# Performance work log

Measured on AMD Instinct MI355X. Metric: run time of the kernel, lower is better.

The kernel has to match this reference:

```python
import jax, jax.numpy as jnp
from jax import lax
import numpy as np

L, G, C = 4, 2, 4  # num_blocks, num_sparsity_groups, num_sparsity_cardinals
IMAGE_MEAN = 0.5
SCALE = 2


def _wn(v, g):
    # weight_norm over dims (1,2,3), g per output channel
    n = jnp.sqrt(jnp.sum(v * v, axis=(1, 2, 3), keepdims=True))
    return (g.reshape(-1, 1, 1, 1) / n) * v


def _conv(x, w, b, pad):
    y = lax.conv_general_dilated(x, w, (1, 1), [(pad, pad), (pad, pad)],
                                 dimension_numbers=('NCHW', 'OIHW', 'NCHW'))
    return y + b[None, :, None, None]


def _dyn_conv(x, v, g, b, mw, mb):
    # sparsity-routed conv: per-sample expert mixture of kernels
    w = _wn(v, g)                                   # [G*out, in, k, k]
    B = x.shape[0]
    logits = x.mean((-1, -2)) @ mw.T + mb           # [B, G*C]
    s = jax.nn.softmax(logits.reshape(B, G, C), axis=1)
    wv = w.reshape(G, C, -1, *w.shape[1:])          # [G, C, D, in, k, k]
    wper = jnp.einsum('bgc,gcdikl->bcdikl', s, wv)
    wper = wper.reshape(B, -1, *w.shape[1:])        # [B, out, in, k, k]
    bper = jnp.einsum('bgc,gcd->bcd', s, b.reshape(G, C, -1)).reshape(B, -1)

    def per_sample(xi, wi, bi):
        yi = lax.conv_general_dilated(xi[None], wi, (1, 1), [(1, 1), (1, 1)],
                                      dimension_numbers=('NCHW', 'OIHW', 'NCHW'))[0]
        return yi + bi[:, None, None]

    return jax.vmap(per_sample)(x, wper, bper)


def _pixel_shuffle(x, r):
    B, Cc, H, W = x.shape
    x = x.reshape(B, Cc // (r * r), r, r, H, W)
    x = x.transpose(0, 1, 4, 2, 5, 3)
    return x.reshape(B, Cc // (r * r), H * r, W * r)


def setup_inputs() -> dict:
    key = jax.random.key(0)
    ks = jax.random.split(key, 16)
    f32 = jnp.float32
    inp = {
        'x': jax.random.uniform(ks[0], (8, 3, 64, 64), dtype=f32),
        'head_v': jax.random.normal(ks[1], (64, 3, 3, 3), dtype=f32) * 0.05,
        'head_g': jnp.ones((64,), f32),
        'head_b': jnp.zeros((64,), f32),
        'b1_v': jax.random.normal(ks[2], (L, 512, 64, 3, 3), dtype=f32) * 0.05,
        'b1_g': jnp.full((L, 512), 2.0, f32),
        'b1_b': jnp.zeros((L, 512), f32),
        'b1_mw': jax.random.normal(ks[3], (L, 8, 64), dtype=f32) * 0.05,
        'b1_mb': jax.random.normal(ks[4], (L, 8), dtype=f32) * 0.05,
        'b2_v': jax.random.normal(ks[5], (L, 128, 256, 3, 3), dtype=f32) * 0.05,
        'b2_g': jnp.full((L, 128), 1.0 / np.sqrt(L), f32),
        'b2_b': jnp.zeros((L, 128), f32),
        'b2_mw': jax.random.normal(ks[6], (L, 8, 256), dtype=f32) * 0.05,
        'b2_mb': jax.random.normal(ks[7], (L, 8), dtype=f32) * 0.05,
        'tail_v': jax.random.normal(ks[8], (12, 64, 3, 3), dtype=f32) * 0.05,
        'tail_g': jnp.ones((12,), f32),
        'tail_b': jnp.zeros((12,), f32),
        'skip_v': jax.random.normal(ks[9], (12, 3, 5, 5), dtype=f32) * 0.05,
        'skip_g': jnp.ones((12,), f32),
        'skip_b': jnp.zeros((12,), f32),
    }
    return inp


def reference(x, head_v, head_g, head_b,
              b1_v, b1_g, b1_b, b1_mw, b1_mb,
              b2_v, b2_g, b2_b, b2_mw, b2_mb,
              tail_v, tail_g, tail_b,
              skip_v, skip_g, skip_b):
    x = x - IMAGE_MEAN
    h = _conv(x, _wn(head_v, head_g), head_b, pad=1)
    for l in range(L):
        r0 = h
        t = _dyn_conv(h, b1_v[l], b1_g[l], b1_b[l], b1_mw[l], b1_mb[l])
        t = jax.nn.relu(t)
        t = _dyn_conv(t, b2_v[l], b2_g[l], b2_b[l], b2_mw[l], b2_mb[l])
        h = t + r0
    body = _conv(h, _wn(tail_v, tail_g), tail_b, pad=1)
    s = _conv(x, _wn(skip_v, skip_g), skip_b, pad=2)
    y = _pixel_shuffle(body + s, SCALE) + IMAGE_MEAN
    return y
```

## Files before the change

### kernel.cpp

```cpp
#include <hip/hip_runtime.h>

typedef __attribute__((ext_vector_type(8))) short bf16x8;
typedef __attribute__((ext_vector_type(4))) float f32x4;
typedef __attribute__((ext_vector_type(4))) unsigned short u16x4;
typedef __attribute__((ext_vector_type(8))) unsigned short u16x8;

__device__ __forceinline__ unsigned short bf16u(float x) {
    unsigned int u = __builtin_bit_cast(unsigned int, x);
    unsigned int r = (u + 0x7fffu + ((u >> 16) & 1u)) >> 16;
    return (unsigned short)r;
}
__device__ __forceinline__ void gll16(const void* g, void* l) {
    __builtin_amdgcn_global_load_lds((const __attribute__((address_space(1))) void*)g,
                                     (__attribute__((address_space(3))) void*)l, 16, 0, 0);
}

__global__ __launch_bounds__(256) void zero_all(unsigned short* __restrict__ hbf,
                                                unsigned short* __restrict__ tbf,
                                                float* __restrict__ sums) {
    int i = blockIdx.x * 256 + threadIdx.x;
    u16x8 z8 = {0, 0, 0, 0, 0, 0, 0, 0};
    if (i < 16640) {
        int chv = i & 7, pb = i >> 3, pos = pb % 260, b = pb / 260;
        int y, x;
        if (pos < 66) { y = 0; x = pos; }
        else if (pos < 132) { y = 65; x = pos - 66; }
        else if (pos < 196) { y = pos - 131; x = 0; }
        else { y = pos - 195; x = 65; }
        *(u16x8*)&hbf[(((size_t)b * 66 + y) * 66 + x) * 64 + chv * 8] = z8;
    } else if (i < 83200) {
        int j = i - 16640;
        int chv = j & 7, pb = j >> 3;
        int pos = pb % 260, bc = pb / 260;
        int y, x;
        if (pos < 66) { y = 0; x = pos; }
        else if (pos < 132) { y = 65; x = pos - 66; }
        else if (pos < 196) { y = pos - 131; x = 0; }
        else { y = pos - 195; x = 65; }
        *(u16x8*)&tbf[(((size_t)bc * 66 + y) * 66 + x) * 64 + chv * 8] = z8;
    } else {
        int k = i - 83200;
        f32x4 z4 = {0.f, 0.f, 0.f, 0.f};
        ((f32x4*)sums)[k] = z4;
    }
}

__global__ __launch_bounds__(256) void wn_all(
    const float* __restrict__ hv, const float* __restrict__ hg, float* __restrict__ hw,
    const float* __restrict__ tv, const float* __restrict__ tg, float* __restrict__ tw,
    const float* __restrict__ kv, const float* __restrict__ kg, float* __restrict__ kw,
    const float* __restrict__ b1v, const float* __restrict__ b1g, float* __restrict__ b1s,
    const float* __restrict__ b2v, const float* __restrict__ b2g, float* __restrict__ b2s) {
    int blk = blockIdx.x;
    const float *v, *g;
    float *outw = nullptr, *outs = nullptr;
    int len, row;
    if (blk < 64)        { v = hv;  g = hg;  outw = hw;  len = 27;   row = blk; }
    else if (blk < 76)   { v = tv;  g = tg;  outw = tw;  len = 576;  row = blk - 64; }
    else if (blk < 88)   { v = kv;  g = kg;  outw = kw;  len = 75;   row = blk - 76; }
    else if (blk < 2136) { v = b1v; g = b1g; outs = b1s; len = 576;  row = blk - 88; }
    else                 { v = b2v; g = b2g; outs = b2s; len = 2304; row = blk - 2136; }

    __shared__ float red[4];
    __shared__ float s_sc;
    const float* vr = v + (size_t)row * len;
    float ss = 0.f;
    for (int i = threadIdx.x; i < len; i += 256) { float a = vr[i]; ss += a * a; }
    for (int o = 32; o > 0; o >>= 1) ss += __shfl_down(ss, o);
    if ((threadIdx.x & 63) == 0) red[threadIdx.x >> 6] = ss;
    __syncthreads();
    if (threadIdx.x == 0) s_sc = g[row] / sqrtf(red[0] + red[1] + red[2] + red[3]);
    __syncthreads();
    float sc = s_sc;
    if (outs) {
        if (threadIdx.x == 0) outs[row] = sc;
    } else {
        float* orow = outw + (size_t)row * len;
        for (int i = threadIdx.x; i < len; i += 256) orow[i] = vr[i] * sc;
    }
}

template <int IC, int GOC, int LGG>
__global__ __launch_bounds__(256) void combine_v2(
    const float* __restrict__ v, const float* __restrict__ scale,
    const float* __restrict__ msum, const float* __restrict__ mw,
    const float* __restrict__ mb, float* __restrict__ s_out,
    unsigned short* __restrict__ wq, int D, int OC) {
    constexpr int ROWF = IC * 9;
    constexpr int KCh = IC / 32;
    constexpr int TOTC = GOC * KCh * 9 * 4;
    __shared__ float lv[2 * GOC * ROWF];
    __shared__ float lg[8], sv8[8];
    int tid = threadIdx.x;
    int b = blockIdx.y, ocg = blockIdx.x * GOC;
    {
        int j = tid >> 5, l32 = tid & 31;
        float part = 0.f;
        for (int i = l32; i < IC; i += 32) part += msum[b * IC + i] * mw[j * IC + i];
        for (int m = 16; m > 0; m >>= 1) part += __shfl_xor(part, m);
        if (l32 == 0) lg[j] = part * (1.f / 4096.f) + mb[j];
    }
    for (int i = tid; i < 2 * GOC * ROWF; i += 256) {
        int r = i / ROWF, jj = i - r * ROWF;
        int oc_r = (r / GOC) * OC + ocg + (r % GOC);
        lv[i] = v[(size_t)oc_r * ROWF + jj] * scale[oc_r];
    }
    __syncthreads();
    if (tid < 8) {
        int g = tid >> 2, c = tid & 3;
        float l0 = lg[c], l1 = lg[4 + c];
        float m = fmaxf(l0, l1);
        float e0 = __expf(l0 - m), e1 = __expf(l1 - m);
        float val = ((g == 0) ? e0 : e1) / (e0 + e1);
        sv8[tid] = val;
        if (blockIdx.x == 0) s_out[b * 8 + tid] = val;
    }
    __syncthreads();
    for (int ci = tid; ci < TOTC; ci += 256) {
        int ml = ci & (GOC - 1);
        int c = ci >> LGG;
        int kg = c & 3, c2 = c >> 2;
        int t = c2 % 9, kc = c2 / 9;
        int oc = ocg + ml;
        int cd = oc / D;
        float s0 = sv8[cd], s1 = sv8[4 + cd];
        const float* p0 = &lv[(size_t)ml * ROWF];
        const float* p1 = &lv[(size_t)(GOC + ml) * ROWF];
        u16x8 pk;
#pragma unroll
        for (int kj = 0; kj < 8; ++kj) {
            int ic9 = (kc * 32 + kg * 8 + kj) * 9 + t;
            pk[kj] = bf16u(s0 * p0[ic9] + s1 * p1[ic9]);
        }
        int ot = oc >> 6, mo = oc & 63;
        size_t w_off = ((((size_t)(b * (OC >> 6) + ot) * KCh + kc) * 9 + t) * 4 + kg) * 512 + mo * 8;
        *(u16x8*)&wq[w_off] = pk;
    }
}

__global__ void tail_repack(const float* __restrict__ tw, unsigned short* __restrict__ wq) {
    int idx = blockIdx.x * 256 + threadIdx.x;
    int kj = idx & 7;
    int tmp = idx >> 3;
    int mo = tmp % 16; tmp /= 16;
    int kg = tmp & 3; tmp >>= 2;
    int t = tmp % 9; tmp /= 9;
    int kc = tmp;
    int ic = kc * 32 + kg * 8 + kj;
    float val = (mo < 12) ? tw[((size_t)mo * 64 + ic) * 9 + t] : 0.f;
    wq[idx] = bf16u(val);
}

template <int IC, int OC, int MT, int WM, int WN, int NR,
          bool RELU, bool RES, bool WF32, bool WBF, int OCR, bool DYNB>
__global__ __launch_bounds__(256) void conv_mfma(
    const unsigned short* __restrict__ in_bf,
    const unsigned short* __restrict__ wq,
    const float* __restrict__ bias_raw, const float* __restrict__ s8, int lgD,
    const float* __restrict__ res, float* __restrict__ out,
    unsigned short* __restrict__ out_bf, float* __restrict__ msum, long wstride) {
    constexpr int KCH = IC / 32;
    constexpr int NRH = NR + 2;
    constexpr int NT = NR * 64;
    constexpr int NF = (NT / 16) / WN;
    constexpr int MW = MT / (16 * WM);
    constexpr int WELEM = 9 * 32 * MT;
    constexpr int SELEM = NRH * 66 * 32;
    constexpr int WCH = WELEM / 8;
    constexpr int SCH = SELEM / 8;
    constexpr int OCB = (OCR % 64 == 0) ? OCR / 64 : 1;

    __shared__ __align__(16) unsigned short S[2][SELEM];
    __shared__ __align__(16) unsigned short W[2][WELEM];
    __shared__ float MRED[WN][MT];

    const int b = blockIdx.z, ot = blockIdx.y;
    const int y0 = blockIdx.x * NR;
    const int tid = threadIdx.x;
    const int lane = tid & 63;
    const int wid = tid >> 6;
    const int wm = wid / WN, wn = wid % WN;
    const int l15 = lane & 15, lk = lane >> 4;
    const int wmo = wm * (MT / WM);
    const int wno = wn * (NT / WN);

    f32x4 acc[MW][NF];
#pragma unroll
    for (int mf = 0; mf < MW; ++mf)
#pragma unroll
        for (int nf = 0; nf < NF; ++nf)
#pragma unroll
            for (int q = 0; q < 4; ++q) acc[mf][nf][q] = 0.f;

    const unsigned short* inb = in_bf + (size_t)b * (IC / 64) * 4356 * 64;
    const unsigned short* wqb = wq + (size_t)b * wstride + (size_t)ot * (KCH * WELEM);

    auto STAGE = [&](int kc, int buf) {
        const unsigned short* wsrc = wqb + (size_t)kc * WELEM;
        for (int i = tid; i < WCH; i += 256)
            gll16(wsrc + i * 8, (char*)W[buf] + i * 16);
        const unsigned short* sb = inb + (size_t)(kc >> 1) * (4356 * 64) + (kc & 1) * 32;
        for (int i = tid; i < SCH; i += 256) {
            int Lz = i ^ ((i >> 3) & 7);
            int lk2 = Lz & 3, cr = Lz >> 2;
            int col = cr % 66, row = cr / 66;
            gll16(sb + ((size_t)(y0 + row) * 66 + col) * 64 + lk2 * 8,
                  (char*)S[buf] + i * 16);
        }
    };

    STAGE(0, 0);
    __syncthreads();
    for (int kc = 0; kc < KCH; ++kc) {
        if (kc + 1 < KCH) STAGE(kc + 1, (kc + 1) & 1);
        const unsigned short* Sb = S[kc & 1];
        const unsigned short* Wb = W[kc & 1];
#pragma unroll
        for (int t = 0; t < 9; ++t) {
            const int dy = t / 3, dx = t % 3;
            bf16x8 a[MW];
#pragma unroll
            for (int mf = 0; mf < MW; ++mf)
                a[mf] = *(const bf16x8*)&Wb[((t * 4 + lk) * MT + wmo + mf * 16 + l15) * 8];
#pragma unroll
            for (int nf = 0; nf < NF; ++nf) {
                int n = wno + nf * 16 + l15;
                int r = n >> 6, c = n & 63;
                int L = ((r + dy) * 66 + (c + dx)) * 4 + lk;
                int P = L ^ ((L >> 3) & 7);
                bf16x8 bv = *(const bf16x8*)((const char*)Sb + P * 16);
#pragma unroll
                for (int mf = 0; mf < MW; ++mf)
                    acc[mf][nf] = __builtin_amdgcn_mfma_f32_16x16x32_bf16(a[mf], bv, acc[mf][nf], 0, 0, 0);
            }
        }
        __syncthreads();
    }

    float msr[MW][4];
#pragma unroll
    for (int mf = 0; mf < MW; ++mf) {
        int ocb = ot * MT + wmo + mf * 16 + lk * 4;
        float bv[4];
#pragma unroll
        for (int q = 0; q < 4; ++q) {
            int oc = ocb + q;
            bv[q] = 0.f;
            if (oc < OCR) {
                if (DYNB) {
                    int c = oc >> lgD;
                    bv[q] = s8[b * 8 + c] * bias_raw[oc] + s8[b * 8 + 4 + c] * bias_raw[OCR + oc];
                } else {
                    bv[q] = bias_raw[oc];
                }
            }
            msr[mf][q] = 0.f;
        }
#pragma unroll
        for (int nf = 0; nf < NF; ++nf) {
            int n = wno + nf * 16 + l15;
            int y = y0 + (n >> 6), x = n & 63;
            float vv[4];
#pragma unroll
            for (int q = 0; q < 4; ++q) {
                int oc = ocb + q;
                float v = 0.f;
                if (oc < OCR) {
                    v = acc[mf][nf][q] + bv[q];
                    if (RELU) v = fmaxf(v, 0.f);
                    size_t o = (((size_t)b * OCR + oc) * 64 + y) * 64 + x;
                    if (RES) v += res[o];
                    if (WF32) out[o] = v;
                    msr[mf][q] += v;
                }
                vv[q] = v;
            }
            if (WBF) {
                u16x4 pk;
#pragma unroll
                for (int q = 0; q < 4; ++q) pk[q] = bf16u(vv[q]);
                if (ocb < OCR)
                    *(u16x4*)&out_bf[((((size_t)b * OCB + (ocb >> 6)) * 66 + y + 1) * 66 +
                                      (x + 1)) * 64 + (ocb & 63)] = pk;
            }
        }
    }
    if (msum) {
#pragma unroll
        for (int mf = 0; mf < MW; ++mf)
#pragma unroll
            for (int q = 0; q < 4; ++q) {
                float vq = msr[mf][q];
                vq += __shfl_xor(vq, 1);
                vq += __shfl_xor(vq, 2);
                vq += __shfl_xor(vq, 4);
                vq += __shfl_xor(vq, 8);
                if (l15 == 0) MRED[wn][wmo + mf * 16 + lk * 4 + q] = vq;
            }
        __syncthreads();
        if (tid < MT) {
            float tot = 0.f;
#pragma unroll
            for (int w2 = 0; w2 < WN; ++w2) tot += MRED[w2][tid];
            atomicAdd(&msum[b * OCR + ot * MT + tid], tot);
        }
    }
}

__global__ __launch_bounds__(256) void head_conv(
    const float* __restrict__ in, const float* __restrict__ w,
    const float* __restrict__ bias, float* __restrict__ out,
    unsigned short* __restrict__ out_bf, float* __restrict__ hsum0) {
    constexpr int OCT = 16, IC = 3;
    __shared__ float s_in[34 * 34];
    __shared__ float s_w[OCT * 9];
    __shared__ float wred[4][OCT];
    int b = blockIdx.z;
    int ocBase = blockIdx.y * OCT;
    int ty0 = (blockIdx.x >> 1) * 32;
    int tx0 = (blockIdx.x & 1) * 32;
    int tid = threadIdx.x;
    int lane = tid & 63, wid = tid >> 6;
    int tx = tid & 15, ty = tid >> 4;

    float acc[OCT][4];
#pragma unroll
    for (int oc = 0; oc < OCT; ++oc)
#pragma unroll
        for (int p = 0; p < 4; ++p) acc[oc][p] = 0.f;

    const float* inb = in + (size_t)b * IC * 4096;
    for (int ic = 0; ic < IC; ++ic) {
        const float* src = inb + (size_t)ic * 4096;
        for (int i = tid; i < 34 * 34; i += 256) {
            int r = i / 34, cc = i % 34;
            int gy = ty0 + r - 1, gx = tx0 + cc - 1;
            float val = 0.f;
            if (gy >= 0 && gy < 64 && gx >= 0 && gx < 64) val = src[gy * 64 + gx] - 0.5f;
            s_in[i] = val;
        }
        for (int i = tid; i < OCT * 9; i += 256) {
            int oc = i / 9, t = i % 9;
            s_w[i] = w[((size_t)(ocBase + oc) * IC + ic) * 9 + t];
        }
        __syncthreads();
        float v[4][4];
#pragma unroll
        for (int r = 0; r < 4; ++r)
#pragma unroll
            for (int cc = 0; cc < 4; ++cc) v[r][cc] = s_in[(2 * ty + r) * 34 + (2 * tx + cc)];
#pragma unroll
        for (int oc = 0; oc < OCT; ++oc) {
#pragma unroll
            for (int ky = 0; ky < 3; ++ky)
#pragma unroll
                for (int kx = 0; kx < 3; ++kx) {
                    float wv = s_w[oc * 9 + ky * 3 + kx];
                    acc[oc][0] += wv * v[ky][kx];
                    acc[oc][1] += wv * v[ky][kx + 1];
                    acc[oc][2] += wv * v[ky + 1][kx];
                    acc[oc][3] += wv * v[ky + 1][kx + 1];
                }
        }
        __syncthreads();
    }
    int py = ty0 + 2 * ty, px = tx0 + 2 * tx;
#pragma unroll
    for (int oc = 0; oc < OCT; ++oc) {
        int og = ocBase + oc;
        float bv = bias[og];
        float osum = 0.f;
#pragma unroll
        for (int p = 0; p < 4; ++p) {
            int dy = p >> 1, dx = p & 1;
            float val = acc[oc][p] + bv;
            osum += val;
            out[(((size_t)b * 64 + og) * 64 + py + dy) * 64 + px + dx] = val;
            out_bf[(((size_t)b * 66 + py + dy + 1) * 66 + (px + dx + 1)) * 64 + og] = bf16u(val);
        }
        for (int m = 1; m < 64; m <<= 1) osum += __shfl_xor(osum, m);
        if (lane == 0) wred[wid][oc] = osum;
    }
    __syncthreads();
    if (tid < OCT)
        atomicAdd(&hsum0[b * 64 + ocBase + tid],
                  wred[0][tid] + wred[1][tid] + wred[2][tid] + wred[3][tid]);
}

__global__ __launch_bounds__(256) void shuffle_skip(
    const float* __restrict__ body, const float* __restrict__ x,
    const float* __restrict__ skw, const float* __restrict__ skb,
    float* __restrict__ out) {
    __shared__ float w[900];
    __shared__ float bb[12];
    int tid = threadIdx.x;
    for (int i = tid; i < 900; i += 256) w[i] = skw[i];
    if (tid < 12) bb[tid] = skb[tid];
    __syncthreads();
    int idx = blockIdx.x * 256 + tid;
    int ox = idx & 127;
    int oy = (idx >> 7) & 127;
    int v = idx >> 14;
    int c = v % 3;
    int b = v / 3;
    int rx = ox & 1, ry = oy & 1;
    int xx = ox >> 1, yy = oy >> 1;
    int ch = c * 4 + ry * 2 + rx;
    float acc = bb[ch];
    for (int ic = 0; ic < 3; ++ic)
        for (int ky = 0; ky < 5; ++ky) {
            int gy = yy + ky - 2;
            if (gy < 0 || gy >= 64) continue;
            for (int kx = 0; kx < 5; ++kx) {
                int gx = xx + kx - 2;
                if (gx < 0 || gx >= 64) continue;
                acc += w[((ch * 3 + ic) * 5 + ky) * 5 + kx] *
                       (x[((size_t)(b * 3 + ic) * 64 + gy) * 64 + gx] - 0.5f);
            }
        }
    size_t src = (((size_t)b * 12 + ch) * 64 + yy) * 64 + xx;
    out[idx] = body[src] + acc + 0.5f;
}

extern "C" void kernel_launch(void* const* d_in, const int* in_sizes, int n_in,
                              void* d_out, int out_size, void* d_ws, size_t ws_size,
                              hipStream_t stream) {
    const float* x      = (const float*)d_in[0];
    const float* head_v = (const float*)d_in[1];
    const float* head_g = (const float*)d_in[2];
    const float* head_b = (const float*)d_in[3];
    const float* b1_v   = (const float*)d_in[4];
    const float* b1_g   = (const float*)d_in[5];
    const float* b1_b   = (const float*)d_in[6];
    const float* b1_mw  = (const float*)d_in[7];
    const float* b1_mb  = (const float*)d_in[8];
    const float* b2_v   = (const float*)d_in[9];
    const float* b2_g   = (const float*)d_in[10];
    const float* b2_b   = (const float*)d_in[11];
    const float* b2_mw  = (const float*)d_in[12];
    const float* b2_mb  = (const float*)d_in[13];
    const float* tail_v = (const float*)d_in[14];
    const float* tail_g = (const float*)d_in[15];
    const float* tail_b = (const float*)d_in[16];
    const float* skip_v = (const float*)d_in[17];
    const float* skip_g = (const float*)d_in[18];
    const float* skip_b = (const float*)d_in[19];

    float* ws = (float*)d_ws;
    size_t off = 0;
    auto alloc = [&](size_t n) { float* p = ws + off; off += (n + 3) & ~(size_t)3; return p; };
    float* head_w = alloc(64 * 27);
    float* tail_w = alloc(12 * 576);
    float* skip_w = alloc(12 * 75);
    float* b1_sc  = alloc(2048);
    float* b2_sc  = alloc(512);
    float* h      = alloc((size_t)8 * 64 * 4096);
    float* sums   = alloc(10240);
    float* sbuf   = alloc(64);
    float* body   = alloc((size_t)8 * 12 * 4096);
    unsigned short* wq1  = (unsigned short*)alloc((size_t)8 * 256 * 576 / 2);
    unsigned short* wq2  = (unsigned short*)alloc((size_t)8 * 64 * 2304 / 2);
    unsigned short* wqt  = (unsigned short*)alloc(9216 / 2);
    unsigned short* h_bf = (unsigned short*)alloc((size_t)8 * 66 * 66 * 64 / 2);
    unsigned short* t_bf = (unsigned short*)alloc((size_t)8 * 4 * 66 * 66 * 64 / 2);
    (void)ws_size; (void)in_sizes; (void)n_in; (void)out_size;

    auto hsum = [&](int l) { return sums + l * 512; };
    auto tsum = [&](int l) { return sums + 2048 + l * 2048; };

    zero_all<<<335, 256, 0, stream>>>(h_bf, t_bf, sums);
    wn_all<<<2648, 256, 0, stream>>>(head_v, head_g, head_w, tail_v, tail_g, tail_w,
                                     skip_v, skip_g, skip_w, b1_v, b1_g, b1_sc,
                                     b2_v, b2_g, b2_sc);
    head_conv<<<dim3(4, 4, 8), 256, 0, stream>>>(x, head_w, head_b, h, h_bf, hsum(0));
    tail_repack<<<36, 256, 0, stream>>>(tail_w, wqt);

    for (int l = 0; l < 4; ++l) {
        combine_v2<64, 4, 2><<<dim3(64, 8), 256, 0, stream>>>(
            b1_v + (size_t)l * 512 * 576, b1_sc + (size_t)l * 512, hsum(l),
            b1_mw + (size_t)l * 8 * 64, b1_mb + l * 8, sbuf, wq1, 64, 256);
        conv_mfma<64, 256, 64, 1, 4, 4, true, false, false, true, 256, true>
            <<<dim3(16, 4, 8), 256, 0, stream>>>(h_bf, wq1, b1_b + (size_t)l * 512, sbuf, 6,
                                                 nullptr, nullptr, t_bf, tsum(l), 147456);
        combine_v2<256, 2, 1><<<dim3(32, 8), 256, 0, stream>>>(
            b2_v + (size_t)l * 128 * 2304, b2_sc + (size_t)l * 128, tsum(l),
            b2_mw + (size_t)l * 8 * 256, b2_mb + l * 8, sbuf, wq2, 16, 64);
        conv_mfma<256, 64, 64, 2, 2, 2, false, true, true, true, 64, true>
            <<<dim3(32, 1, 8), 256, 0, stream>>>(t_bf, wq2, b2_b + (size_t)l * 128, sbuf, 4,
                                                 h, h, h_bf, (l < 3) ? hsum(l + 1) : nullptr,
                                                 147456);
    }

    conv_mfma<64, 16, 16, 1, 4, 4, false, false, true, false, 12, false>
        <<<dim3(16, 1, 8), 256, 0, stream>>>(h_bf, wqt, tail_b, nullptr, 0,
                                             nullptr, body, nullptr, nullptr, 0);
    shuffle_skip<<<1536, 256, 0, stream>>>(body, x, skip_w, skip_b, (float*)d_out);
}
```

Measured before the change: 365.6 us.

## Load conv weights directly from global into registers with prefetch, widen conv2 blocks

Drops LDS staging of the weight tiles in conv_mfma. Each lane now reads its A fragments straight from global memory into registers, prefetching the next tap's fragment while the current tap's MFMAs run. This cuts shared-memory footprint and LDS traffic, and launch bounds now request higher occupancy. The second conv runs with 512 threads (2x4 waves) so each wave covers fewer columns. The cost is uncached, latency-exposed global weight loads repeated per wave, in place of one shared copy per block.

```diff
diff --git a/kernel.cpp b/kernel.cpp
--- a/kernel.cpp
+++ b/kernel.cpp
@@ -153,12 +153,14 @@
 
 template <int IC, int OC, int MT, int WM, int WN, int NR,
           bool RELU, bool RES, bool WF32, bool WBF, int OCR, bool DYNB>
-__global__ __launch_bounds__(256) void conv_mfma(
+__global__ __launch_bounds__(WM * WN * 64, ((WM * WN * 64) == 256) ? 3 : 2)
+void conv_mfma(
     const unsigned short* __restrict__ in_bf,
     const unsigned short* __restrict__ wq,
     const float* __restrict__ bias_raw, const float* __restrict__ s8, int lgD,
     const float* __restrict__ res, float* __restrict__ out,
     unsigned short* __restrict__ out_bf, float* __restrict__ msum, long wstride) {
+    constexpr int THREADS = WM * WN * 64;
     constexpr int KCH = IC / 32;
     constexpr int NRH = NR + 2;
     constexpr int NT = NR * 64;
@@ -166,12 +168,10 @@
     constexpr int MW = MT / (16 * WM);
     constexpr int WELEM = 9 * 32 * MT;
     constexpr int SELEM = NRH * 66 * 32;
-    constexpr int WCH = WELEM / 8;
     constexpr int SCH = SELEM / 8;
     constexpr int OCB = (OCR % 64 == 0) ? OCR / 64 : 1;
 
     __shared__ __align__(16) unsigned short S[2][SELEM];
-    __shared__ __align__(16) unsigned short W[2][WELEM];
     __shared__ float MRED[WN][MT];
 
     const int b = blockIdx.z, ot = blockIdx.y;
@@ -194,13 +194,11 @@
 
     const unsigned short* inb = in_bf + (size_t)b * (IC / 64) * 4356 * 64;
     const unsigned short* wqb = wq + (size_t)b * wstride + (size_t)ot * (KCH * WELEM);
-
-    auto STAGE = [&](int kc, int buf) {
-        const unsigned short* wsrc = wqb + (size_t)kc * WELEM;
-        for (int i = tid; i < WCH; i += 256)
-            gll16(wsrc + i * 8, (char*)W[buf] + i * 16);
+    const unsigned short* wqa = wqb + (size_t)lk * (MT * 8) + (size_t)(wmo + l15) * 8;
+
+    auto STAGE_S = [&](int kc, int buf) {
         const unsigned short* sb = inb + (size_t)(kc >> 1) * (4356 * 64) + (kc & 1) * 32;
-        for (int i = tid; i < SCH; i += 256) {
+        for (int i = tid; i < SCH; i += THREADS) {
             int Lz = i ^ ((i >> 3) & 7);
             int lk2 = Lz & 3, cr = Lz >> 2;
             int col = cr % 66, row = cr / 66;
@@ -209,19 +207,27 @@
         }
     };
 
-    STAGE(0, 0);
+    STAGE_S(0, 0);
     __syncthreads();
     for (int kc = 0; kc < KCH; ++kc) {
-        if (kc + 1 < KCH) STAGE(kc + 1, (kc + 1) & 1);
+        if (kc + 1 < KCH) STAGE_S(kc + 1, (kc + 1) & 1);
         const unsigned short* Sb = S[kc & 1];
-        const unsigned short* Wb = W[kc & 1];
+        const unsigned short* wk = wqa + (size_t)kc * 9 * (4 * MT * 8);
+        bf16x8 aN[MW];
+#pragma unroll
+        for (int mf = 0; mf < MW; ++mf)
+            aN[mf] = *(const bf16x8*)(wk + mf * 128);
 #pragma unroll
         for (int t = 0; t < 9; ++t) {
             const int dy = t / 3, dx = t % 3;
-            bf16x8 a[MW];
-#pragma unroll
-            for (int mf = 0; mf < MW; ++mf)
-                a[mf] = *(const bf16x8*)&Wb[((t * 4 + lk) * MT + wmo + mf * 16 + l15) * 8];
+            bf16x8 aC[MW];
+#pragma unroll
+            for (int mf = 0; mf < MW; ++mf) aC[mf] = aN[mf];
+            if (t < 8) {
+#pragma unroll
+                for (int mf = 0; mf < MW; ++mf)
+                    aN[mf] = *(const bf16x8*)(wk + (t + 1) * (4 * MT * 8) + mf * 128);
+            }
 #pragma unroll
             for (int nf = 0; nf < NF; ++nf) {
                 int n = wno + nf * 16 + l15;
@@ -231,7 +237,7 @@
                 bf16x8 bv = *(const bf16x8*)((const char*)Sb + P * 16);
 #pragma unroll
                 for (int mf = 0; mf < MW; ++mf)
-                    acc[mf][nf] = __builtin_amdgcn_mfma_f32_16x16x32_bf16(a[mf], bv, acc[mf][nf], 0, 0, 0);
+                    acc[mf][nf] = __builtin_amdgcn_mfma_f32_16x16x32_bf16(aC[mf], bv, acc[mf][nf], 0, 0, 0);
             }
         }
         __syncthreads();
@@ -485,8 +491,8 @@
         combine_v2<256, 2, 1><<<dim3(32, 8), 256, 0, stream>>>(
             b2_v + (size_t)l * 128 * 2304, b2_sc + (size_t)l * 128, tsum(l),
             b2_mw + (size_t)l * 8 * 256, b2_mb + l * 8, sbuf, wq2, 16, 64);
-        conv_mfma<256, 64, 64, 2, 2, 2, false, true, true, true, 64, true>
-            <<<dim3(32, 1, 8), 256, 0, stream>>>(t_bf, wq2, b2_b + (size_t)l * 128, sbuf, 4,
+        conv_mfma<256, 64, 64, 2, 4, 2, false, true, true, true, 64, true>
+            <<<dim3(32, 1, 8), 512, 0, stream>>>(t_bf, wq2, b2_b + (size_t)l * 128, sbuf, 4,
                                                  h, h, h_bf, (l < 3) ? hsum(l + 1) : nullptr,
                                                  147456);
     }
```

Result: faster. 356.4 us (-2.5%).
